# Kernel optimization log

Hardware: AMD Instinct MI355X
Metric: run time of the kernel (lower is better)

The kernel has to match this reference:

```python
import math
import jax, jax.numpy as jnp
import numpy as np

B, T, D = 32, 2048, 512
FACTOR = 2
TOP_K = int(FACTOR * math.log(T))  # = 15, static (T is static under jit)


def setup_inputs() -> dict:
    key = jax.random.key(0)
    ks = jax.random.split(key, 11)
    s = 1.0 / math.sqrt(D)
    return {
        "query": jax.random.normal(ks[0], (B, T, D), jnp.float32),
        "key_in": jax.random.normal(ks[1], (B, T, D), jnp.float32),
        "value": jax.random.normal(ks[2], (B, T, D), jnp.float32),
        "Wq": jax.random.normal(ks[3], (D, D), jnp.float32) * s,
        "bq": jnp.zeros((D,), jnp.float32),
        "Wk": jax.random.normal(ks[4], (D, D), jnp.float32) * s,
        "bk": jnp.zeros((D,), jnp.float32),
        "Wv": jax.random.normal(ks[5], (D, D), jnp.float32) * s,
        "bv": jnp.zeros((D,), jnp.float32),
        "Wo": jax.random.normal(ks[6], (D, D), jnp.float32) * s,
        "bo": jnp.zeros((D,), jnp.float32),
    }


def reference(query, key_in, value, Wq, bq, Wk, bk, Wv, bv, Wo, bo):
    # Linear projections (query/key/value lengths are equal here, so no trimming)
    q = query @ Wq + bq      # [B, T, D]
    k = key_in @ Wk + bk     # [B, T, D]
    v = value @ Wv + bv      # [B, T, D]

    # FFT cross-correlation along the time axis
    qf = jnp.fft.rfft(q, axis=1)
    kf = jnp.fft.rfft(k, axis=1)
    attn_weights = jnp.fft.irfft(qf * jnp.conj(kf), n=T, axis=1)  # [B, T, D]

    # Top-k delay selection on the feature-mean autocorrelation
    autocorr_mean = attn_weights.mean(axis=-1)           # [B, T]
    _, topk_delays = jax.lax.top_k(autocorr_mean, TOP_K)  # [B, K] int32

    # Sum of circularly-rolled values over the top-k delays.
    # tf.roll(v, s, 0): out[t] = v[(t - s) mod T]; accumulate via scan over K
    def body(acc, d):  # d: [B] delays for this k
        rolled = jax.vmap(lambda vb, db: jnp.roll(vb, db, axis=0))(v, d)
        return acc + rolled, None

    rolled_sum, _ = jax.lax.scan(body, jnp.zeros_like(v), topk_delays.T)  # [B, T, D]

    # Softmax over the feature axis (independent of k in the original loop)
    soft_attn = jax.nn.softmax(attn_weights, axis=-1)    # [B, T, D]
    attn_output = rolled_sum * soft_attn                 # [B, T, D]

    return attn_output @ Wo + bo
```

## Files before the change

### kernel.cpp

```cpp
#include <hip/hip_runtime.h>

#define NFFT 2048
#define LDK 40
#define FFT_PAD(p) ((p) + ((p) >> 5))

typedef __attribute__((ext_vector_type(8))) short bf16x8;
typedef __attribute__((ext_vector_type(4))) float f32x4;

__device__ __forceinline__ unsigned short f2bf_rne(float x) {
  unsigned u = __float_as_uint(x);
  return (unsigned short)((u + 0x7fffu + ((u >> 16) & 1u)) >> 16);
}
__device__ __forceinline__ float bf2f(unsigned short h) {
  return __uint_as_float(((unsigned)h) << 16);
}

__global__ __launch_bounds__(256) void wsplit_kernel(
    const float* __restrict__ W0, const float* __restrict__ W1,
    const float* __restrict__ W2, const float* __restrict__ W3,
    unsigned short* __restrict__ out) {
  __shared__ float tile[32][33];
  const float* W = (blockIdx.z == 0) ? W0
                   : (blockIdx.z == 1) ? W1
                   : (blockIdx.z == 2) ? W2 : W3;
  unsigned short* hi = out + (size_t)blockIdx.z * 524288;
  unsigned short* lo = hi + 262144;
  const int k0 = blockIdx.x * 32, n0 = blockIdx.y * 32;
  const int c = threadIdx.x & 31, r = threadIdx.x >> 5;
#pragma unroll
  for (int p = 0; p < 4; p++)
    tile[r + 8 * p][c] = W[(size_t)(k0 + r + 8 * p) * 512 + n0 + c];
  __syncthreads();
#pragma unroll
  for (int p = 0; p < 4; p++) {
    int nn = r + 8 * p;
    float x = tile[c][nn];
    unsigned u = __float_as_uint(x);
    unsigned short h = (unsigned short)(u >> 16);
    float hf = __uint_as_float(u & 0xffff0000u);
    unsigned short l = f2bf_rne(x - hf);
    hi[(size_t)(n0 + nn) * 512 + k0 + c] = h;
    lo[(size_t)(n0 + nn) * 512 + k0 + c] = l;
  }
}

__global__ __launch_bounds__(256) void proj_gemm_split(
    const float* __restrict__ X, const unsigned short* __restrict__ WThi,
    const unsigned short* __restrict__ WTlo, const float* __restrict__ bias,
    float* __restrict__ YT) {
  __shared__ __align__(16) unsigned short Wh[128 * LDK];
  __shared__ __align__(16) unsigned short Wl[128 * LDK];
  __shared__ __align__(16) unsigned short Xh[128 * LDK];
  __shared__ __align__(16) unsigned short Xl[128 * LDK];
  const int tid = threadIdx.x;
  const int n0 = blockIdx.x * 128;
  const int b = blockIdx.y >> 4;
  const int t0 = (blockIdx.y & 15) * 128;
  const int w = tid >> 6, l = tid & 63;
  const int wn = (w & 1) * 64;
  const int wt = (w >> 1) * 64;
  const int fr = l & 15;
  const int fk = (l >> 4) * 8;

  f32x4 acc[4][4];
#pragma unroll
  for (int i = 0; i < 4; i++)
#pragma unroll
    for (int j = 0; j < 4; j++) acc[i][j] = (f32x4)0.f;

  const int srow = tid >> 1, scol = (tid & 1) * 16;
  const float* Xg = X + ((size_t)(b * 2048 + t0 + srow)) * 512 + scol;
  const unsigned short* Whg = WThi + ((size_t)(n0 + srow)) * 512 + scol;
  const unsigned short* Wlg = WTlo + ((size_t)(n0 + srow)) * 512 + scol;
  unsigned short* XhL = &Xh[srow * LDK + scol];
  unsigned short* XlL = &Xl[srow * LDK + scol];
  unsigned short* WhL = &Wh[srow * LDK + scol];
  unsigned short* WlL = &Wl[srow * LDK + scol];

  for (int k0 = 0; k0 < 512; k0 += 32) {
    float xv[16];
    *(float4*)&xv[0] = *(const float4*)&Xg[k0];
    *(float4*)&xv[4] = *(const float4*)&Xg[k0 + 4];
    *(float4*)&xv[8] = *(const float4*)&Xg[k0 + 8];
    *(float4*)&xv[12] = *(const float4*)&Xg[k0 + 12];
    uint4 wh0 = *(const uint4*)&Whg[k0];
    uint4 wh1 = *(const uint4*)&Whg[k0 + 8];
    uint4 wl0 = *(const uint4*)&Wlg[k0];
    uint4 wl1 = *(const uint4*)&Wlg[k0 + 8];
    union { unsigned short us[16]; uint4 q[2]; } hb, lb;
#pragma unroll
    for (int i = 0; i < 16; i++) {
      unsigned u = __float_as_uint(xv[i]);
      hb.us[i] = (unsigned short)(u >> 16);
      float hf = __uint_as_float(u & 0xffff0000u);
      lb.us[i] = f2bf_rne(xv[i] - hf);
    }
    __syncthreads();
    *(uint4*)&XhL[0] = hb.q[0];
    *(uint4*)&XhL[8] = hb.q[1];
    *(uint4*)&XlL[0] = lb.q[0];
    *(uint4*)&XlL[8] = lb.q[1];
    *(uint4*)&WhL[0] = wh0;
    *(uint4*)&WhL[8] = wh1;
    *(uint4*)&WlL[0] = wl0;
    *(uint4*)&WlL[8] = wl1;
    __syncthreads();
    bf16x8 ah[4], al[4], bh[4], bl[4];
#pragma unroll
    for (int i = 0; i < 4; i++) {
      ah[i] = *(const bf16x8*)&Wh[(wn + 16 * i + fr) * LDK + fk];
      al[i] = *(const bf16x8*)&Wl[(wn + 16 * i + fr) * LDK + fk];
      bh[i] = *(const bf16x8*)&Xh[(wt + 16 * i + fr) * LDK + fk];
      bl[i] = *(const bf16x8*)&Xl[(wt + 16 * i + fr) * LDK + fk];
    }
#pragma unroll
    for (int i = 0; i < 4; i++)
#pragma unroll
      for (int j = 0; j < 4; j++) {
        acc[i][j] = __builtin_amdgcn_mfma_f32_16x16x32_bf16(ah[i], bh[j],
                                                            acc[i][j], 0, 0, 0);
        acc[i][j] = __builtin_amdgcn_mfma_f32_16x16x32_bf16(al[i], bh[j],
                                                            acc[i][j], 0, 0, 0);
        acc[i][j] = __builtin_amdgcn_mfma_f32_16x16x32_bf16(ah[i], bl[j],
                                                            acc[i][j], 0, 0, 0);
      }
  }
  const size_t obase = (size_t)b * 512 * 2048;
#pragma unroll
  for (int i = 0; i < 4; i++) {
#pragma unroll
    for (int r = 0; r < 4; r++) {
      int n = n0 + wn + 16 * i + (l >> 4) * 4 + r;
      float bsc = bias[n];
      size_t row = obase + (size_t)n * 2048 + t0 + wt + (l & 15);
#pragma unroll
      for (int j = 0; j < 4; j++) YT[row + 16 * j] = acc[i][j][r] + bsc;
    }
  }
}

__global__ __launch_bounds__(256) void gemm_bf16_vproj(
    const float* __restrict__ X, const unsigned short* __restrict__ WThi,
    const float* __restrict__ bias, unsigned short* __restrict__ Vbf) {
  __shared__ __align__(16) unsigned short Ws[128 * LDK];
  __shared__ __align__(16) unsigned short Xs[128 * LDK];
  const int tid = threadIdx.x;
  const int n0 = blockIdx.x * 128;
  const int b = blockIdx.y >> 4;
  const int t0 = (blockIdx.y & 15) * 128;
  const int w = tid >> 6, l = tid & 63;
  const int wr = (w & 1) * 64;
  const int wc = (w >> 1) * 64;
  const int fr = l & 15, fk = (l >> 4) * 8;

  f32x4 acc[4][4];
#pragma unroll
  for (int i = 0; i < 4; i++)
#pragma unroll
    for (int j = 0; j < 4; j++) acc[i][j] = (f32x4)0.f;

  const int srow = tid >> 1, scol = (tid & 1) * 16;
  const float* Xg = X + ((size_t)(b * 2048 + t0 + srow)) * 512 + scol;
  const unsigned short* Wg = WThi + ((size_t)(n0 + srow)) * 512 + scol;
  unsigned short* XsL = &Xs[srow * LDK + scol];
  unsigned short* WsL = &Ws[srow * LDK + scol];

  for (int k0 = 0; k0 < 512; k0 += 32) {
    float xv[16];
    *(float4*)&xv[0] = *(const float4*)&Xg[k0];
    *(float4*)&xv[4] = *(const float4*)&Xg[k0 + 4];
    *(float4*)&xv[8] = *(const float4*)&Xg[k0 + 8];
    *(float4*)&xv[12] = *(const float4*)&Xg[k0 + 12];
    uint4 w0 = *(const uint4*)&Wg[k0];
    uint4 w1 = *(const uint4*)&Wg[k0 + 8];
    union { unsigned short us[16]; uint4 q[2]; } hb;
#pragma unroll
    for (int i = 0; i < 16; i++) hb.us[i] = f2bf_rne(xv[i]);
    __syncthreads();
    *(uint4*)&XsL[0] = hb.q[0];
    *(uint4*)&XsL[8] = hb.q[1];
    *(uint4*)&WsL[0] = w0;
    *(uint4*)&WsL[8] = w1;
    __syncthreads();
    bf16x8 af[4], bf[4];
#pragma unroll
    for (int i = 0; i < 4; i++) {
      af[i] = *(const bf16x8*)&Xs[(wr + 16 * i + fr) * LDK + fk];
      bf[i] = *(const bf16x8*)&Ws[(wc + 16 * i + fr) * LDK + fk];
    }
#pragma unroll
    for (int i = 0; i < 4; i++)
#pragma unroll
      for (int j = 0; j < 4; j++)
        acc[i][j] = __builtin_amdgcn_mfma_f32_16x16x32_bf16(af[i], bf[j],
                                                            acc[i][j], 0, 0, 0);
  }
  float bj[4];
#pragma unroll
  for (int j = 0; j < 4; j++) bj[j] = bias[n0 + wc + 16 * j + (l & 15)];
#pragma unroll
  for (int i = 0; i < 4; i++) {
#pragma unroll
    for (int r = 0; r < 4; r++) {
      int t = t0 + wr + 16 * i + (l >> 4) * 4 + r;
      unsigned short* vrow = Vbf + ((size_t)(b * 2048 + t)) * 512;
#pragma unroll
      for (int j = 0; j < 4; j++) {
        int d = n0 + wc + 16 * j + (l & 15);
        vrow[d] = f2bf_rne(acc[i][j][r] + bj[j]);
      }
    }
  }
}

__global__ __launch_bounds__(256) void gemm_bf16_out(
    const unsigned short* __restrict__ Abf,
    const unsigned short* __restrict__ WThi, const float* __restrict__ bias,
    float* __restrict__ Y) {
  __shared__ __align__(16) unsigned short Ws[128 * LDK];
  __shared__ __align__(16) unsigned short Xs[128 * LDK];
  const int tid = threadIdx.x;
  const int n0 = blockIdx.x * 128;
  const int b = blockIdx.y >> 4;
  const int t0 = (blockIdx.y & 15) * 128;
  const int w = tid >> 6, l = tid & 63;
  const int wr = (w & 1) * 64;
  const int wc = (w >> 1) * 64;
  const int fr = l & 15, fk = (l >> 4) * 8;

  f32x4 acc[4][4];
#pragma unroll
  for (int i = 0; i < 4; i++)
#pragma unroll
    for (int j = 0; j < 4; j++) acc[i][j] = (f32x4)0.f;

  const int srow = tid >> 1, scol = (tid & 1) * 16;
  const unsigned short* Ag = Abf + ((size_t)(b * 2048 + t0 + srow)) * 512 + scol;
  const unsigned short* Wg = WThi + ((size_t)(n0 + srow)) * 512 + scol;
  unsigned short* XsL = &Xs[srow * LDK + scol];
  unsigned short* WsL = &Ws[srow * LDK + scol];

  for (int k0 = 0; k0 < 512; k0 += 32) {
    uint4 a0 = *(const uint4*)&Ag[k0];
    uint4 a1 = *(const uint4*)&Ag[k0 + 8];
    uint4 w0 = *(const uint4*)&Wg[k0];
    uint4 w1 = *(const uint4*)&Wg[k0 + 8];
    __syncthreads();
    *(uint4*)&XsL[0] = a0;
    *(uint4*)&XsL[8] = a1;
    *(uint4*)&WsL[0] = w0;
    *(uint4*)&WsL[8] = w1;
    __syncthreads();
    bf16x8 af[4], bf[4];
#pragma unroll
    for (int i = 0; i < 4; i++) {
      af[i] = *(const bf16x8*)&Xs[(wr + 16 * i + fr) * LDK + fk];
      bf[i] = *(const bf16x8*)&Ws[(wc + 16 * i + fr) * LDK + fk];
    }
#pragma unroll
    for (int i = 0; i < 4; i++)
#pragma unroll
      for (int j = 0; j < 4; j++)
        acc[i][j] = __builtin_amdgcn_mfma_f32_16x16x32_bf16(af[i], bf[j],
                                                            acc[i][j], 0, 0, 0);
  }
  float bj[4];
#pragma unroll
  for (int j = 0; j < 4; j++) bj[j] = bias[n0 + wc + 16 * j + (l & 15)];
#pragma unroll
  for (int i = 0; i < 4; i++) {
#pragma unroll
    for (int r = 0; r < 4; r++) {
      int t = t0 + wr + 16 * i + (l >> 4) * 4 + r;
      float* yrow = Y + ((size_t)(b * 2048 + t)) * 512;
#pragma unroll
      for (int j = 0; j < 4; j++) {
        int n = n0 + wc + 16 * j + (l & 15);
        yrow[n] = acc[i][j][r] + bj[j];
      }
    }
  }
}

__device__ __forceinline__ float2 cadd(float2 a, float2 b) {
  return make_float2(a.x + b.x, a.y + b.y);
}
__device__ __forceinline__ float2 csub(float2 a, float2 b) {
  return make_float2(a.x - b.x, a.y - b.y);
}
__device__ __forceinline__ float2 cmulf(float2 a, float2 b) {
  return make_float2(a.x * b.x - a.y * b.y, a.x * b.y + a.y * b.x);
}
template <int SGN>
__device__ __forceinline__ float2 mul_i(float2 a) {
  return (SGN < 0) ? make_float2(a.y, -a.x) : make_float2(-a.y, a.x);
}

template <int SGN>
__device__ __forceinline__ void dft4(float2 v[4]) {
  float2 b0 = cadd(v[0], v[2]);
  float2 b2 = csub(v[0], v[2]);
  float2 b1 = cadd(v[1], v[3]);
  float2 b3 = mul_i<SGN>(csub(v[1], v[3]));
  v[0] = cadd(b0, b1);
  v[2] = csub(b0, b1);
  v[1] = cadd(b2, b3);
  v[3] = csub(b2, b3);
}

template <int SGN>
__device__ __forceinline__ void dft8(float2 v[8]) {
  const float C = 0.70710678118654752f;
  float2 e[4], o[4];
#pragma unroll
  for (int i = 0; i < 4; i++) {
    e[i] = cadd(v[i], v[i + 4]);
    o[i] = csub(v[i], v[i + 4]);
  }
  {
    float s = o[1].x, t = o[1].y;
    o[1] = (SGN < 0) ? make_float2(C * (s + t), C * (t - s))
                     : make_float2(C * (s - t), C * (s + t));
  }
  o[2] = mul_i<SGN>(o[2]);
  {
    float s = o[3].x, t = o[3].y;
    o[3] = (SGN < 0) ? make_float2(C * (t - s), -C * (s + t))
                     : make_float2(-C * (s + t), C * (s - t));
  }
  dft4<SGN>(e);
  dft4<SGN>(o);
  v[0] = e[0]; v[2] = e[1]; v[4] = e[2]; v[6] = e[3];
  v[1] = o[0]; v[3] = o[1]; v[5] = o[2]; v[7] = o[3];
}

__device__ __forceinline__ void twiddle8_pair(float2 vz[8], float2 vw[8],
                                              float ang) {
  float2 T;
  __sincosf(ang, &T.y, &T.x);
  float2 t = T;
  vz[1] = cmulf(vz[1], t);
  vw[1] = cmulf(vw[1], t);
#pragma unroll
  for (int r = 2; r < 8; r++) {
    t = cmulf(t, T);
    vz[r] = cmulf(vz[r], t);
    vw[r] = cmulf(vw[r], t);
  }
}
__device__ __forceinline__ void twiddle8_one(float2 v[8], float ang) {
  float2 T;
  __sincosf(ang, &T.y, &T.x);
  float2 t = T;
  v[1] = cmulf(v[1], t);
#pragma unroll
  for (int r = 2; r < 8; r++) {
    t = cmulf(t, T);
    v[r] = cmulf(v[r], t);
  }
}

__global__ __launch_bounds__(256) void fft_correlate(
    float* __restrict__ qT, const float* __restrict__ kT) {
  __shared__ float2 ldsZ[2112];
  __shared__ float2 ldsW[2112];
  const int b = blockIdx.x;
  const int d0 = blockIdx.y * 2;
  const int tid = threadIdx.x;
  const size_t base = ((size_t)b * 512 + d0) * 2048;

  const float W1 = -6.28318530717958647692f / 2048.f;
  const int j2 = tid & 31, j3 = tid & 3;
  const int s1 = tid >> 5, s2 = tid >> 2;
  const int f1 = ((tid & 7) << 6) | (tid & 56) | (tid >> 6);
  const int pt = tid + (tid >> 5);
  const int b2 = 264 * s1 + j2;
  const int b3 = 33 * s2 + j3;

  float2 vz[8], vw[8];
#pragma unroll
  for (int r = 0; r < 8; r++) {
    int t = tid + (r << 8);
    vz[r] = make_float2(qT[base + t], qT[base + 2048 + t]);
    vw[r] = make_float2(kT[base + t], kT[base + 2048 + t]);
  }

  dft8<-1>(vz);
  dft8<-1>(vw);
  twiddle8_pair(vz, vw, W1 * (float)tid);
#pragma unroll
  for (int r = 0; r < 8; r++) {
    ldsZ[pt + 264 * r] = vz[r];
    ldsW[pt + 264 * r] = vw[r];
  }
  __syncthreads();
#pragma unroll
  for (int m = 0; m < 8; m++) {
    vz[m] = ldsZ[b2 + 33 * m];
    vw[m] = ldsW[b2 + 33 * m];
  }
  dft8<-1>(vz);
  dft8<-1>(vw);
  twiddle8_pair(vz, vw, (W1 * 8.f) * (float)j2);
#pragma unroll
  for (int r = 0; r < 8; r++) {
    ldsZ[b2 + 33 * r] = vz[r];
    ldsW[b2 + 33 * r] = vw[r];
  }
  __syncthreads();
#pragma unroll
  for (int m = 0; m < 8; m++) {
    vz[m] = ldsZ[b3 + 4 * m];
    vw[m] = ldsW[b3 + 4 * m];
  }
  dft8<-1>(vz);
  dft8<-1>(vw);
  twiddle8_pair(vz, vw, (W1 * 64.f) * (float)j3);
#pragma unroll
  for (int r = 0; r < 8; r++) {
    ldsZ[b3 + 4 * r] = vz[r];
    ldsW[b3 + 4 * r] = vw[r];
  }
  __syncthreads();
  {
    float2 za[4], zb[4], wa[4], wb[4];
    const int pb = f1 << 2;
#pragma unroll
    for (int c = 0; c < 4; c++) {
      za[c] = ldsZ[FFT_PAD(pb + c)];
      zb[c] = ldsZ[FFT_PAD(pb + 16 + c)];
      wa[c] = ldsW[FFT_PAD(pb + c)];
      wb[c] = ldsW[FFT_PAD(pb + 16 + c)];
    }
    dft4<-1>(za);
    dft4<-1>(zb);
    dft4<-1>(wa);
    dft4<-1>(wb);
    __syncthreads();
#pragma unroll
    for (int c = 0; c < 4; c++) {
      ldsZ[pt + 528 * c] = za[c];
      ldsZ[pt + 264 + 528 * c] = zb[c];
      ldsW[pt + 528 * c] = wa[c];
      ldsW[pt + 264 + 528 * c] = wb[c];
    }
  }
  __syncthreads();

  float2 G[8];
#pragma unroll
  for (int r = 0; r < 8; r++) {
    int f = tid + (r << 8);
    int fn = (NFFT - f) & (NFFT - 1);
    float2 Zf = ldsZ[pt + 264 * r], Zn = ldsZ[FFT_PAD(fn)];
    float2 Wf = ldsW[pt + 264 * r], Wn = ldsW[FFT_PAD(fn)];
    float A1x = Zf.x + Zn.x, A1y = Zf.y - Zn.y;
    float B1x = Wf.x + Wn.x, B1y = Wn.y - Wf.y;
    float A2x = Zf.x - Zn.x, A2y = Zf.y + Zn.y;
    float B2x = Wf.x - Wn.x, B2y = -Wf.y - Wn.y;
    float p1x = A1x * B1x - A1y * B1y;
    float p1y = A1x * B1y + A1y * B1x;
    float p2x = A2x * B2x - A2y * B2y;
    float p2y = A2x * B2y + A2y * B2x;
    G[r] = make_float2(0.25f * (p1x - p2y), 0.25f * (p1y + p2x));
    (void)f;
  }
  __syncthreads();

  dft8<1>(G);
  twiddle8_one(G, (-W1) * (float)tid);
#pragma unroll
  for (int r = 0; r < 8; r++) ldsZ[pt + 264 * r] = G[r];
  __syncthreads();
#pragma unroll
  for (int m = 0; m < 8; m++) G[m] = ldsZ[b2 + 33 * m];
  dft8<1>(G);
  twiddle8_one(G, (-W1 * 8.f) * (float)j2);
#pragma unroll
  for (int r = 0; r < 8; r++) ldsZ[b2 + 33 * r] = G[r];
  __syncthreads();
#pragma unroll
  for (int m = 0; m < 8; m++) G[m] = ldsZ[b3 + 4 * m];
  dft8<1>(G);
  twiddle8_one(G, (-W1 * 64.f) * (float)j3);
#pragma unroll
  for (int r = 0; r < 8; r++) ldsZ[b3 + 4 * r] = G[r];
  __syncthreads();
  {
    float2 za[4], zb[4];
    const int pb = f1 << 2;
#pragma unroll
    for (int c = 0; c < 4; c++) {
      za[c] = ldsZ[FFT_PAD(pb + c)];
      zb[c] = ldsZ[FFT_PAD(pb + 16 + c)];
    }
    dft4<1>(za);
    dft4<1>(zb);
    const float scale = 1.0f / (float)NFFT;
#pragma unroll
    for (int c = 0; c < 4; c++) {
      int ta = tid + (c << 9);
      int tb = ta + 256;
      qT[base + ta] = za[c].x * scale;
      qT[base + 2048 + ta] = za[c].y * scale;
      qT[base + tb] = zb[c].x * scale;
      qT[base + 2048 + tb] = zb[c].y * scale;
    }
  }
}

__global__ __launch_bounds__(256) void colstats_kernel(
    const float* __restrict__ attnT, float* __restrict__ mean,
    float2* __restrict__ stats) {
  const int b = blockIdx.x;
  const int t = blockIdx.y * 256 + threadIdx.x;
  const size_t base = (size_t)b * 512 * 2048 + t;
  float sum = 0.f, m = -1e30f, s = 0.f;
  for (int d = 0; d < 512; d++) {
    float a = attnT[base + (size_t)d * 2048];
    sum += a;
    float mn = fmaxf(m, a);
    s = s * __expf(m - mn) + __expf(a - mn);
    m = mn;
  }
  mean[b * 2048 + t] = sum * (1.f / 512.f);
  stats[b * 2048 + t] = make_float2(m, s);
}

__global__ __launch_bounds__(256) void topk_kernel(
    const float* __restrict__ mean, int* __restrict__ delays) {
  __shared__ float vals[2048];
  __shared__ float sv[256];
  __shared__ int si[256];
  const int b = blockIdx.x, tid = threadIdx.x;
#pragma unroll
  for (int r = 0; r < 8; r++)
    vals[tid + (r << 8)] = mean[b * 2048 + tid + (r << 8)];
  __syncthreads();
  for (int k = 0; k < 15; k++) {
    float bv = -1e30f;
    int bi = 1 << 30;
#pragma unroll
    for (int r = 0; r < 8; r++) {
      int i = (r << 8) + tid;
      float v = vals[i];
      if (v > bv || (v == bv && i < bi)) { bv = v; bi = i; }
    }
    sv[tid] = bv;
    si[tid] = bi;
    __syncthreads();
    for (int off = 128; off > 0; off >>= 1) {
      if (tid < off) {
        float v2 = sv[tid + off];
        int i2 = si[tid + off];
        if (v2 > sv[tid] || (v2 == sv[tid] && i2 < si[tid])) {
          sv[tid] = v2;
          si[tid] = i2;
        }
      }
      __syncthreads();
    }
    if (tid == 0) {
      delays[b * 15 + k] = si[0];
      vals[si[0]] = -1e30f;
    }
    __syncthreads();
  }
}

__global__ __launch_bounds__(256) void ctx_kernel(
    const float* __restrict__ attnT, const unsigned short* __restrict__ vbf,
    const float2* __restrict__ stats, const int* __restrict__ delays,
    unsigned short* __restrict__ ctx) {
  __shared__ float atile[64][65];
  __shared__ int dly[15];
  const int lin = blockIdx.x;
  const int g = lin >> 8;
  const int r = lin & 255;
  const int b = g * 8 + (r & 7);
  const int tb = (r >> 3) * 64;
  const int tid = threadIdx.x;
  if (tid < 15) dly[tid] = delays[b * 15 + tid];
  __syncthreads();

  const int tl = tid >> 2;
  const int dq = (tid & 3) * 16;
  const int tq = (tid & 3) * 4;
  const int t = tb + tl;
  const float2 st = stats[b * 2048 + t];
  const float m = st.x, inv_s = 1.f / st.y;

  int rowoff[15];
#pragma unroll
  for (int k = 0; k < 15; k++)
    rowoff[k] = ((t - dly[k]) & 2047) * 512;

  const size_t vbase = (size_t)b * 2048 * 512;
  const size_t abase = (size_t)b * 512 * 2048;

  for (int d0 = 0; d0 < 512; d0 += 64) {
    __syncthreads();
#pragma unroll
    for (int tt = 0; tt < 4; tt++) {
      float4 a4 = *(const float4*)&attnT[abase + (size_t)(d0 + tl) * 2048 +
                                         tb + tt * 16 + tq];
      atile[tt * 16 + tq + 0][tl] = a4.x;
      atile[tt * 16 + tq + 1][tl] = a4.y;
      atile[tt * 16 + tq + 2][tl] = a4.z;
      atile[tt * 16 + tq + 3][tl] = a4.w;
    }
    __syncthreads();

    float rolled[16];
#pragma unroll
    for (int i = 0; i < 16; i++) rolled[i] = 0.f;
#pragma unroll
    for (int k = 0; k < 15; k++) {
      const uint4* vp = (const uint4*)(vbf + vbase + rowoff[k] + d0 + dq);
      uint4 v0 = vp[0], v1 = vp[1];
      unsigned uu[8] = {v0.x, v0.y, v0.z, v0.w, v1.x, v1.y, v1.z, v1.w};
#pragma unroll
      for (int w = 0; w < 8; w++) {
        rolled[2 * w + 0] += __uint_as_float(uu[w] << 16);
        rolled[2 * w + 1] += __uint_as_float(uu[w] & 0xffff0000u);
      }
    }

    union { unsigned short us[16]; uint4 q[2]; } ob;
#pragma unroll
    for (int i = 0; i < 16; i++) {
      float a = atile[tl][dq + i];
      float p = __expf(a - m) * inv_s;
      ob.us[i] = f2bf_rne(p * rolled[i]);
    }
    uint4* op = (uint4*)(ctx + vbase + (size_t)t * 512 + d0 + dq);
    op[0] = ob.q[0];
    op[1] = ob.q[1];
  }
}

extern "C" void kernel_launch(void* const* d_in, const int* in_sizes, int n_in,
                              void* d_out, int out_size, void* d_ws,
                              size_t ws_size, hipStream_t stream) {
  const float* query = (const float*)d_in[0];
  const float* key_in = (const float*)d_in[1];
  const float* value = (const float*)d_in[2];
  const float* Wq = (const float*)d_in[3];
  const float* bq = (const float*)d_in[4];
  const float* Wk = (const float*)d_in[5];
  const float* bk = (const float*)d_in[6];
  const float* Wv = (const float*)d_in[7];
  const float* bv = (const float*)d_in[8];
  const float* Wo = (const float*)d_in[9];
  const float* bo = (const float*)d_in[10];
  float* out = (float*)d_out;

  float* ws = (float*)d_ws;
  const size_t SZ = (size_t)32 * 512 * 2048;
  float* qT = ws;
  float* kT = ws + SZ;
  unsigned short* vbf = (unsigned short*)(ws + SZ);
  unsigned short* ctxbf = (unsigned short*)(ws + SZ + SZ / 2);
  unsigned short* wbuf = (unsigned short*)(ws + 2 * SZ);
  float* mean = ws + 2 * SZ + 1048576;
  float2* stats = (float2*)(ws + 2 * SZ + 1048576 + 65536);
  int* delays = (int*)(ws + 2 * SZ + 1048576 + 65536 + 131072);

  const unsigned short* wq_hi = wbuf + 0 * 524288;
  const unsigned short* wq_lo = wq_hi + 262144;
  const unsigned short* wk_hi = wbuf + 1 * 524288;
  const unsigned short* wk_lo = wk_hi + 262144;
  const unsigned short* wv_hi = wbuf + 2 * 524288;
  const unsigned short* wo_hi = wbuf + 3 * 524288;

  wsplit_kernel<<<dim3(16, 16, 4), 256, 0, stream>>>(Wq, Wk, Wv, Wo, wbuf);

  proj_gemm_split<<<dim3(4, 512), 256, 0, stream>>>(query, wq_hi, wq_lo, bq, qT);
  proj_gemm_split<<<dim3(4, 512), 256, 0, stream>>>(key_in, wk_hi, wk_lo, bk, kT);

  fft_correlate<<<dim3(32, 256), 256, 0, stream>>>(qT, kT);

  gemm_bf16_vproj<<<dim3(4, 512), 256, 0, stream>>>(value, wv_hi, bv, vbf);

  colstats_kernel<<<dim3(32, 8), 256, 0, stream>>>(qT, mean, stats);
  topk_kernel<<<32, 256, 0, stream>>>(mean, delays);
  ctx_kernel<<<1024, 256, 0, stream>>>(qT, vbf, stats, delays, ctxbf);

  gemm_bf16_out<<<dim3(4, 512), 256, 0, stream>>>(ctxbf, wo_hi, bo, out);
}
```

Baseline: 1.056 ms.

## Prefetch next K-tile into registers and remap GEMM blocks for XCD locality

All four GEMM kernels now load the next K-slice of global data into registers after the shared-memory barrier, so global latency overlaps the MFMA work on the current slice. The launch grid is flattened to 1D and decoded so that the four N-blocks sharing one X row tile run on the same XCD, which should improve L2 reuse of the activation tile. This raises register pressure from keeping the prefetch buffers live, which could lower occupancy.

```diff
diff --git a/kernel.cpp b/kernel.cpp
--- a/kernel.cpp
+++ b/kernel.cpp
@@ -13,6 +13,17 @@
 }
 __device__ __forceinline__ float bf2f(unsigned short h) {
   return __uint_as_float(((unsigned)h) << 16);
+}
+
+__device__ __forceinline__ void gemm_decode(int lin, int& n0, int& b,
+                                            int& t0) {
+  const int xcd = lin & 7;
+  const int j = lin >> 3;
+  const int nblk = j & 3;
+  const int y = (j >> 2) * 8 + xcd;
+  n0 = nblk * 128;
+  b = y >> 4;
+  t0 = (y & 15) * 128;
 }
 
 __global__ __launch_bounds__(256) void wsplit_kernel(
@@ -53,9 +64,8 @@
   __shared__ __align__(16) unsigned short Xh[128 * LDK];
   __shared__ __align__(16) unsigned short Xl[128 * LDK];
   const int tid = threadIdx.x;
-  const int n0 = blockIdx.x * 128;
-  const int b = blockIdx.y >> 4;
-  const int t0 = (blockIdx.y & 15) * 128;
+  int n0, b, t0;
+  gemm_decode(blockIdx.x, n0, b, t0);
   const int w = tid >> 6, l = tid & 63;
   const int wn = (w & 1) * 64;
   const int wt = (w >> 1) * 64;
@@ -77,16 +87,18 @@
   unsigned short* WhL = &Wh[srow * LDK + scol];
   unsigned short* WlL = &Wl[srow * LDK + scol];
 
+  float xv[16];
+  uint4 wh0, wh1, wl0, wl1;
+  *(float4*)&xv[0] = *(const float4*)&Xg[0];
+  *(float4*)&xv[4] = *(const float4*)&Xg[4];
+  *(float4*)&xv[8] = *(const float4*)&Xg[8];
+  *(float4*)&xv[12] = *(const float4*)&Xg[12];
+  wh0 = *(const uint4*)&Whg[0];
+  wh1 = *(const uint4*)&Whg[8];
+  wl0 = *(const uint4*)&Wlg[0];
+  wl1 = *(const uint4*)&Wlg[8];
+
   for (int k0 = 0; k0 < 512; k0 += 32) {
-    float xv[16];
-    *(float4*)&xv[0] = *(const float4*)&Xg[k0];
-    *(float4*)&xv[4] = *(const float4*)&Xg[k0 + 4];
-    *(float4*)&xv[8] = *(const float4*)&Xg[k0 + 8];
-    *(float4*)&xv[12] = *(const float4*)&Xg[k0 + 12];
-    uint4 wh0 = *(const uint4*)&Whg[k0];
-    uint4 wh1 = *(const uint4*)&Whg[k0 + 8];
-    uint4 wl0 = *(const uint4*)&Wlg[k0];
-    uint4 wl1 = *(const uint4*)&Wlg[k0 + 8];
     union { unsigned short us[16]; uint4 q[2]; } hb, lb;
 #pragma unroll
     for (int i = 0; i < 16; i++) {
@@ -105,6 +117,17 @@
     *(uint4*)&WlL[0] = wl0;
     *(uint4*)&WlL[8] = wl1;
     __syncthreads();
+    const int k1 = k0 + 32;
+    if (k1 < 512) {
+      *(float4*)&xv[0] = *(const float4*)&Xg[k1];
+      *(float4*)&xv[4] = *(const float4*)&Xg[k1 + 4];
+      *(float4*)&xv[8] = *(const float4*)&Xg[k1 + 8];
+      *(float4*)&xv[12] = *(const float4*)&Xg[k1 + 12];
+      wh0 = *(const uint4*)&Whg[k1];
+      wh1 = *(const uint4*)&Whg[k1 + 8];
+      wl0 = *(const uint4*)&Wlg[k1];
+      wl1 = *(const uint4*)&Wlg[k1 + 8];
+    }
     bf16x8 ah[4], al[4], bh[4], bl[4];
 #pragma unroll
     for (int i = 0; i < 4; i++) {
@@ -145,9 +168,8 @@
   __shared__ __align__(16) unsigned short Ws[128 * LDK];
   __shared__ __align__(16) unsigned short Xs[128 * LDK];
   const int tid = threadIdx.x;
-  const int n0 = blockIdx.x * 128;
-  const int b = blockIdx.y >> 4;
-  const int t0 = (blockIdx.y & 15) * 128;
+  int n0, b, t0;
+  gemm_decode(blockIdx.x, n0, b, t0);
   const int w = tid >> 6, l = tid & 63;
   const int wr = (w & 1) * 64;
   const int wc = (w >> 1) * 64;
@@ -165,14 +187,16 @@
   unsigned short* XsL = &Xs[srow * LDK + scol];
   unsigned short* WsL = &Ws[srow * LDK + scol];
 
+  float xv[16];
+  uint4 w0, w1;
+  *(float4*)&xv[0] = *(const float4*)&Xg[0];
+  *(float4*)&xv[4] = *(const float4*)&Xg[4];
+  *(float4*)&xv[8] = *(const float4*)&Xg[8];
+  *(float4*)&xv[12] = *(const float4*)&Xg[12];
+  w0 = *(const uint4*)&Wg[0];
+  w1 = *(const uint4*)&Wg[8];
+
   for (int k0 = 0; k0 < 512; k0 += 32) {
-    float xv[16];
-    *(float4*)&xv[0] = *(const float4*)&Xg[k0];
-    *(float4*)&xv[4] = *(const float4*)&Xg[k0 + 4];
-    *(float4*)&xv[8] = *(const float4*)&Xg[k0 + 8];
-    *(float4*)&xv[12] = *(const float4*)&Xg[k0 + 12];
-    uint4 w0 = *(const uint4*)&Wg[k0];
-    uint4 w1 = *(const uint4*)&Wg[k0 + 8];
     union { unsigned short us[16]; uint4 q[2]; } hb;
 #pragma unroll
     for (int i = 0; i < 16; i++) hb.us[i] = f2bf_rne(xv[i]);
@@ -182,6 +206,15 @@
     *(uint4*)&WsL[0] = w0;
     *(uint4*)&WsL[8] = w1;
     __syncthreads();
+    const int k1 = k0 + 32;
+    if (k1 < 512) {
+      *(float4*)&xv[0] = *(const float4*)&Xg[k1];
+      *(float4*)&xv[4] = *(const float4*)&Xg[k1 + 4];
+      *(float4*)&xv[8] = *(const float4*)&Xg[k1 + 8];
+      *(float4*)&xv[12] = *(const float4*)&Xg[k1 + 12];
+      w0 = *(const uint4*)&Wg[k1];
+      w1 = *(const uint4*)&Wg[k1 + 8];
+    }
     bf16x8 af[4], bf[4];
 #pragma unroll
     for (int i = 0; i < 4; i++) {
@@ -220,9 +253,8 @@
   __shared__ __align__(16) unsigned short Ws[128 * LDK];
   __shared__ __align__(16) unsigned short Xs[128 * LDK];
   const int tid = threadIdx.x;
-  const int n0 = blockIdx.x * 128;
-  const int b = blockIdx.y >> 4;
-  const int t0 = (blockIdx.y & 15) * 128;
+  int n0, b, t0;
+  gemm_decode(blockIdx.x, n0, b, t0);
   const int w = tid >> 6, l = tid & 63;
   const int wr = (w & 1) * 64;
   const int wc = (w >> 1) * 64;
@@ -240,17 +272,26 @@
   unsigned short* XsL = &Xs[srow * LDK + scol];
   unsigned short* WsL = &Ws[srow * LDK + scol];
 
+  uint4 a0, a1, w0, w1;
+  a0 = *(const uint4*)&Ag[0];
+  a1 = *(const uint4*)&Ag[8];
+  w0 = *(const uint4*)&Wg[0];
+  w1 = *(const uint4*)&Wg[8];
+
   for (int k0 = 0; k0 < 512; k0 += 32) {
-    uint4 a0 = *(const uint4*)&Ag[k0];
-    uint4 a1 = *(const uint4*)&Ag[k0 + 8];
-    uint4 w0 = *(const uint4*)&Wg[k0];
-    uint4 w1 = *(const uint4*)&Wg[k0 + 8];
     __syncthreads();
     *(uint4*)&XsL[0] = a0;
     *(uint4*)&XsL[8] = a1;
     *(uint4*)&WsL[0] = w0;
     *(uint4*)&WsL[8] = w1;
     __syncthreads();
+    const int k1 = k0 + 32;
+    if (k1 < 512) {
+      a0 = *(const uint4*)&Ag[k1];
+      a1 = *(const uint4*)&Ag[k1 + 8];
+      w0 = *(const uint4*)&Wg[k1];
+      w1 = *(const uint4*)&Wg[k1 + 8];
+    }
     bf16x8 af[4], bf[4];
 #pragma unroll
     for (int i = 0; i < 4; i++) {
@@ -675,16 +716,16 @@
 
   wsplit_kernel<<<dim3(16, 16, 4), 256, 0, stream>>>(Wq, Wk, Wv, Wo, wbuf);
 
-  proj_gemm_split<<<dim3(4, 512), 256, 0, stream>>>(query, wq_hi, wq_lo, bq, qT);
-  proj_gemm_split<<<dim3(4, 512), 256, 0, stream>>>(key_in, wk_hi, wk_lo, bk, kT);
+  proj_gemm_split<<<2048, 256, 0, stream>>>(query, wq_hi, wq_lo, bq, qT);
+  proj_gemm_split<<<2048, 256, 0, stream>>>(key_in, wk_hi, wk_lo, bk, kT);
 
   fft_correlate<<<dim3(32, 256), 256, 0, stream>>>(qT, kT);
 
-  gemm_bf16_vproj<<<dim3(4, 512), 256, 0, stream>>>(value, wv_hi, bv, vbf);
+  gemm_bf16_vproj<<<2048, 256, 0, stream>>>(value, wv_hi, bv, vbf);
 
   colstats_kernel<<<dim3(32, 8), 256, 0, stream>>>(qT, mean, stats);
   topk_kernel<<<32, 256, 0, stream>>>(mean, delays);
   ctx_kernel<<<1024, 256, 0, stream>>>(qT, vbf, stats, delays, ctxbf);
 
-  gemm_bf16_out<<<dim3(4, 512), 256, 0, stream>>>(ctxbf, wo_hi, bo, out);
-}
+  gemm_bf16_out<<<2048, 256, 0, stream>>>(ctxbf, wo_hi, bo, out);
+}
```

New measurement: 984.5 us. 6.8% less time.
